# Performance work log

Hardware: AMD Instinct MI355X
Metric: run time of the kernel (lower is better)

The kernel has to match this reference:

```python
import jax, jax.numpy as jnp
import numpy as np

N_NODES = 100000
N_EDGES = 3200000
IN_C, HID_C, OUT_C = 64, 128, 64


def gcn_conv(x, src, dst, W, b, n):
    """PyG GCNConv: h = x @ W; out[d] += norm(e) * h[s]; norm = deg^-1/2[s]*deg^-1/2[d].
    src/dst already include self-loops."""
    h = x @ W  # [N, out_c]
    deg = jax.ops.segment_sum(jnp.ones_like(dst, dtype=h.dtype), dst, num_segments=n)
    dinv = jnp.where(deg > 0, jax.lax.rsqrt(deg), 0.0)
    norm = dinv[src] * dinv[dst]  # [E]
    msg = h[src] * norm[:, None]  # [E, out_c] -- dominant memory traffic
    return jax.ops.segment_sum(msg, dst, num_segments=n) + b


def setup_inputs() -> dict:
    key = jax.random.key(0)
    k1, k2, k3, k4 = jax.random.split(key, 4)
    x = jax.random.normal(k1, (N_NODES, IN_C), dtype=jnp.float32)
    edge_index = jax.random.randint(k2, (2, N_EDGES), 0, N_NODES, dtype=jnp.int64)
    W1 = jax.random.normal(k3, (IN_C, HID_C), dtype=jnp.float32) / np.sqrt(IN_C)
    b1 = jnp.zeros((HID_C,), dtype=jnp.float32)
    W2 = jax.random.normal(k4, (HID_C, OUT_C), dtype=jnp.float32) / np.sqrt(HID_C)
    b2 = jnp.zeros((OUT_C,), dtype=jnp.float32)
    return {"x": x, "edge_index": edge_index, "W1": W1, "b1": b1, "W2": W2, "b2": b2}


def reference(x, edge_index, W1, b1, W2, b2):
    n = x.shape[0]
    loops = jnp.arange(n, dtype=edge_index.dtype)  # self-loops, as PyG GCNConv adds
    src = jnp.concatenate([edge_index[0], loops])
    dst = jnp.concatenate([edge_index[1], loops])
    h = gcn_conv(x, src, dst, W1, b1, n)
    h = jax.nn.relu(h)
    out = gcn_conv(h, src, dst, W2, b2, n)
    return out
```

## Files before the change

### kernel.cpp

```cpp
#include <hip/hip_runtime.h>
#include <math.h>


#define IN_C 64
#define HID_C 128
#define OUT_C 64
#define BSHIFT 9
#define BW (1 << BSHIFT)
#define NPB 512

typedef __attribute__((ext_vector_type(8))) short bf16x8;
typedef __attribute__((ext_vector_type(4))) float f32x4;
typedef __attribute__((ext_vector_type(2))) float v2f;

__device__ __forceinline__ unsigned short f2bf(float f) {
  unsigned u = __float_as_uint(f);
  return (unsigned short)((u + 0x7FFF + ((u >> 16) & 1)) >> 16);
}
__device__ __forceinline__ v2f cvt2(unsigned u) {
  v2f r;
  r.x = __uint_as_float(u << 16);
  r.y = __uint_as_float(u & 0xFFFF0000u);
  return r;
}
__device__ __forceinline__ unsigned pack2(v2f v) {
  return ((unsigned)f2bf(v.y) << 16) | f2bf(v.x);
}


__global__ __launch_bounds__(256) void k_part1(const int* __restrict__ ei, int e, int n,
    int nb, int* __restrict__ pcnt,
    const float* __restrict__ W1, const float* __restrict__ W2,
    unsigned short* __restrict__ Wt1, unsigned short* __restrict__ Wt2,
    unsigned short* __restrict__ xs_zero, unsigned short* __restrict__ h2s_zero) {
  extern __shared__ int lh[];
  const int t = threadIdx.x;
  if (blockIdx.x >= NPB) {
    int bb = blockIdx.x - NPB;
    if (bb == 32) {
      if (t < 64) { xs_zero[t] = 0; h2s_zero[t] = 0; }
      return;
    }
    int i = bb * 256 + t;
    if (i < IN_C * HID_C) {
      int k = i >> 7, c = i & (HID_C - 1);
      Wt1[c * IN_C + k] = f2bf(W1[i]);
    }
    if (i < HID_C * OUT_C) {
      int k = i >> 6, c = i & (OUT_C - 1);
      Wt2[c * HID_C + k] = f2bf(W2[i]);
    }
    return;
  }
  __shared__ int sflag;
  if (t == 0) sflag = 0;
  for (int i = t; i < nb; i += 256) lh[i] = 0;
  __syncthreads();
  const int chunk = (e + NPB - 1) / NPB;
  const int lo = blockIdx.x * chunk;
  const int hi = min(lo + chunk, e);
  {
    int lim = min(hi, lo + 512);
    int f = 0;
    for (int i = lo + t; i < lim; i += 256)
      if (ei[2 * i + 1] != 0) f = 1;
    if (f) sflag = 1;
  }
  __syncthreads();
  const int f = sflag;
  for (int i = lo + t; i < hi; i += 256) {
    int d;
    if (f) d = __builtin_nontemporal_load(&ei[e + i]);
    else   d = (int)__builtin_nontemporal_load(&((const long long*)ei)[e + i]);
    d = min(max(d, 0), n - 1);
    atomicAdd(&lh[d >> BSHIFT], 1);
  }
  __syncthreads();
  for (int i = t; i < nb; i += 256) pcnt[(size_t)i * NPB + blockIdx.x] = lh[i];
}


__global__ __launch_bounds__(256) void k_bscan(int* __restrict__ pcnt,
    int* __restrict__ btot) {
  __shared__ int ws[256];
  const int b = blockIdx.x;
  const int t = threadIdx.x;
  int* row = pcnt + (size_t)b * NPB;
  int2 v = ((int2*)row)[t];
  int s0 = v.x;
  int s1 = s0 + v.y;
  ws[t] = s1;
  __syncthreads();
  for (int off = 1; off < 256; off <<= 1) {
    int u = (t >= off) ? ws[t - off] : 0;
    __syncthreads();
    ws[t] += u;
    __syncthreads();
  }
  int base = (t == 0) ? 0 : ws[t - 1];
  ((int2*)row)[t] = make_int2(base, base + s0);
  if (t == 255) btot[b] = ws[255];
}


__global__ __launch_bounds__(256) void k_part2(const int* __restrict__ ei, int e, int n,
    int nb, const int* __restrict__ pcnt, const int* __restrict__ btot,
    unsigned* __restrict__ ebuf) {
  __shared__ int se[256];
  __shared__ int base_l[256];
  __shared__ int cur[256];
  __shared__ int sflag;
  const int t = threadIdx.x;
  if (t == 0) sflag = 0;
  se[t] = (t < nb) ? btot[t] : 0;
  __syncthreads();
  for (int off = 1; off < 256; off <<= 1) {
    int u = (t >= off) ? se[t - off] : 0;
    __syncthreads();
    se[t] += u;
    __syncthreads();
  }
  if (t < nb) {
    int eb = (t == 0) ? 0 : se[t - 1];
    base_l[t] = eb + pcnt[(size_t)t * NPB + blockIdx.x];
    cur[t] = 0;
  }
  const int chunk = (e + NPB - 1) / NPB;
  const int lo = blockIdx.x * chunk;
  const int hi = min(lo + chunk, e);
  {
    int lim = min(hi, lo + 512);
    int f = 0;
    for (int i = lo + t; i < lim; i += 256)
      if (ei[2 * i + 1] != 0) f = 1;
    if (f) sflag = 1;
  }
  __syncthreads();
  const int f = sflag;
  for (int i = lo + t; i < hi; i += 256) {
    int s, d;
    if (f) {
      s = __builtin_nontemporal_load(&ei[i]);
      d = __builtin_nontemporal_load(&ei[e + i]);
    } else {
      s = (int)__builtin_nontemporal_load(&((const long long*)ei)[i]);
      d = (int)__builtin_nontemporal_load(&((const long long*)ei)[e + i]);
    }
    s = min(max(s, 0), n - 1);
    d = min(max(d, 0), n - 1);
    int b = d >> BSHIFT;
    int slot = atomicAdd(&cur[b], 1);
    ebuf[base_l[b] + slot] = ((unsigned)(d & (BW - 1)) << 23) | (unsigned)s;
  }
}


__global__ __launch_bounds__(1024) void k_finalize(const unsigned* __restrict__ ebuf,
    const int* __restrict__ btot, const float* __restrict__ x,
    unsigned short* __restrict__ xs, int n, int nb,
    int* __restrict__ row_ptr, float* __restrict__ dinv, int* __restrict__ col) {
  __shared__ int se[256], sc[256];
  __shared__ int ldeg[BW];
  __shared__ int lofs[BW];
  __shared__ int lcur[BW];
  __shared__ float sdv[BW];
  __shared__ int wsum[256];
  const int b = blockIdx.x;
  const int t = threadIdx.x;
  const int T = 1024;
  int bc = 0, nodes = 0;
  if (t < nb) {
    bc = btot[t];
    nodes = min(BW, n - t * BW);
  }
  if (t < 256) { se[t] = bc; sc[t] = bc + nodes; }
  __syncthreads();
  for (int off = 1; off < 256; off <<= 1) {
    int ve = 0, vc = 0;
    if (t < 256 && t >= off) { ve = se[t - off]; vc = sc[t - off]; }
    __syncthreads();
    if (t < 256) { se[t] += ve; sc[t] += vc; }
    __syncthreads();
  }
  const int eb = (b == 0) ? 0 : se[b - 1];
  const int ee = se[b];
  const int cb = (b == 0) ? 0 : sc[b - 1];
  const int lo = b * BW;
  const int nn = min(BW, n - lo);
  for (int k = t; k < BW; k += T) ldeg[k] = 0;
  __syncthreads();
  for (int k = t; k < nn; k += T) ldeg[k] = 1;
  __syncthreads();
  for (int j = eb + t; j < ee; j += T) {
    int dl = (int)(ebuf[j] >> 23);
    atomicAdd(&ldeg[dl], 1);
  }
  __syncthreads();
  int p0 = 0, p1 = 0;
  if (t < 256) {
    p0 = ldeg[2 * t]; p1 = ldeg[2 * t + 1];
    wsum[t] = p0 + p1;
  }
  __syncthreads();
  for (int off = 1; off < 256; off <<= 1) {
    int v = 0;
    if (t < 256 && t >= off) v = wsum[t - off];
    __syncthreads();
    if (t < 256) wsum[t] += v;
    __syncthreads();
  }
  if (t < 256) {
    int pb = (t == 0) ? 0 : wsum[t - 1];
    lofs[2 * t] = pb;
    lofs[2 * t + 1] = pb + p0;
  }
  __syncthreads();
  for (int k = t; k < nn; k += T) {
    int base = cb + lofs[k];
    float dv = rsqrtf((float)ldeg[k]);
    row_ptr[lo + k] = base;
    dinv[lo + k] = dv;
    sdv[k] = dv;
    col[base] = lo + k;
    lcur[k] = lofs[k] + 1;
  }
  if (b == nb - 1 && t == 0) row_ptr[n] = sc[nb - 1];
  __syncthreads();
  for (int j = eb + t; j < ee; j += T) {
    unsigned pk = ebuf[j];
    int s = (int)(pk & 0x7FFFFF);
    int dl = (int)(pk >> 23);
    int p = atomicAdd(&lcur[dl], 1);
    col[cb + p] = s;
  }
  const float4* x4 = (const float4*)x;
  for (int idx = t; idx < nn * 16; idx += T) {
    int row = idx >> 4, q = idx & 15;
    float sc2 = sdv[row];
    float4 v = x4[(size_t)(lo + row) * 16 + q];
    ushort4 o;
    o.x = f2bf(v.x * sc2); o.y = f2bf(v.y * sc2);
    o.z = f2bf(v.z * sc2); o.w = f2bf(v.w * sc2);
    ((ushort4*)xs)[(size_t)(lo + row) * 16 + q] = o;
  }
}


template<bool BIAS, bool OUT_BF16>
__global__ __launch_bounds__(256) void k_agg(const unsigned short* __restrict__ feat,
    const int* __restrict__ row_ptr, const int* __restrict__ col,
    const float* __restrict__ dinv, const float* __restrict__ bias,
    void* __restrict__ outv, int n) {
  const int wid = threadIdx.x >> 6;
  const int lane = threadIdx.x & 63;
  const int es = lane >> 3;
  const int c8 = lane & 7;
  const int d = blockIdx.x * 4 + wid;
  if (d >= n) return;
  const int beg = row_ptr[d], end = row_ptr[d + 1];
  const uint4* f16 = (const uint4*)feat;
  const int rem = end - beg - es;
  const int c = (rem > 0) ? ((rem + 7) >> 3) : 0;
  const int last = end - 1;
  v2f a0 = {0.f, 0.f}, a1 = {0.f, 0.f}, a2 = {0.f, 0.f}, a3 = {0.f, 0.f};
  for (int g = 0; g < c; g += 4) {
    int j0 = beg + es + 8 * g;
    int i0 = col[j0];
    int i1 = col[min(j0 + 8, last)];
    int i2 = col[min(j0 + 16, last)];
    int i3 = col[min(j0 + 24, last)];
    if (g + 1 >= c) i1 = n;
    if (g + 2 >= c) i2 = n;
    if (g + 3 >= c) i3 = n;
    uint4 u0 = f16[(size_t)i0 * 8 + c8];
    uint4 u1 = f16[(size_t)i1 * 8 + c8];
    uint4 u2 = f16[(size_t)i2 * 8 + c8];
    uint4 u3 = f16[(size_t)i3 * 8 + c8];
    a0 += cvt2(u0.x) + cvt2(u1.x) + cvt2(u2.x) + cvt2(u3.x);
    a1 += cvt2(u0.y) + cvt2(u1.y) + cvt2(u2.y) + cvt2(u3.y);
    a2 += cvt2(u0.z) + cvt2(u1.z) + cvt2(u2.z) + cvt2(u3.z);
    a3 += cvt2(u0.w) + cvt2(u1.w) + cvt2(u2.w) + cvt2(u3.w);
  }
#pragma unroll
  for (int off = 8; off <= 32; off <<= 1) {
    v2f o0, o1, o2, o3;
    o0.x = __shfl_xor(a0.x, off); o0.y = __shfl_xor(a0.y, off);
    o1.x = __shfl_xor(a1.x, off); o1.y = __shfl_xor(a1.y, off);
    o2.x = __shfl_xor(a2.x, off); o2.y = __shfl_xor(a2.y, off);
    o3.x = __shfl_xor(a3.x, off); o3.y = __shfl_xor(a3.y, off);
    a0 += o0; a1 += o1; a2 += o2; a3 += o3;
  }
  if (es == 0) {
    float sc = dinv[d];
    v2f vs = {sc, sc};
    a0 *= vs; a1 *= vs; a2 *= vs; a3 *= vs;
    if (BIAS) {
      const v2f* b2v = (const v2f*)bias;
      a0 += b2v[c8 * 4 + 0]; a1 += b2v[c8 * 4 + 1];
      a2 += b2v[c8 * 4 + 2]; a3 += b2v[c8 * 4 + 3];
    }
    if (OUT_BF16) {
      uint4 o;
      o.x = pack2(a0); o.y = pack2(a1); o.z = pack2(a2); o.w = pack2(a3);
      ((uint4*)outv)[(size_t)d * 8 + c8] = o;
    } else {
      float4* o4 = (float4*)outv;
      o4[(size_t)d * 16 + c8 * 2]     = make_float4(a0.x, a0.y, a1.x, a1.y);
      o4[(size_t)d * 16 + c8 * 2 + 1] = make_float4(a2.x, a2.y, a3.x, a3.y);
    }
  }
}


__global__ __launch_bounds__(256) void k_mlp(const unsigned short* __restrict__ A1,
    const unsigned short* __restrict__ Wt1, const unsigned short* __restrict__ Wt2,
    const float* __restrict__ b1, const float* __restrict__ dinv,
    unsigned short* __restrict__ h2s, int M) {
  __shared__ unsigned short sA[16 * 136];
  const int wv = threadIdx.x >> 6;
  const int lane = threadIdx.x & 63;
  const int m = lane & 15;
  const int q = lane >> 4;
  const int r0 = blockIdx.x * 16;
  const int ra = min(r0 + m, M - 1);
  f32x4 acc0 = {0.f, 0.f, 0.f, 0.f}, acc1 = {0.f, 0.f, 0.f, 0.f};
#pragma unroll
  for (int kt = 0; kt < IN_C; kt += 32) {
    bf16x8 a  = *(const bf16x8*)&A1[(size_t)ra * IN_C + kt + q * 8];
    bf16x8 p  = *(const bf16x8*)&Wt1[(size_t)(wv * 16 + m) * IN_C + kt + q * 8];
    bf16x8 p2 = *(const bf16x8*)&Wt1[(size_t)((wv + 4) * 16 + m) * IN_C + kt + q * 8];
    acc0 = __builtin_amdgcn_mfma_f32_16x16x32_bf16(a, p, acc0, 0, 0, 0);
    acc1 = __builtin_amdgcn_mfma_f32_16x16x32_bf16(a, p2, acc1, 0, 0, 0);
  }
  float dv[4];
#pragma unroll
  for (int i = 0; i < 4; i++) dv[i] = dinv[min(r0 + q * 4 + i, M - 1)];
  {
    int c = wv * 16 + m;
    float bv = b1[c];
#pragma unroll
    for (int i = 0; i < 4; i++)
      sA[(q * 4 + i) * 136 + c] = f2bf(fmaxf(acc0[i] + bv, 0.f) * dv[i]);
    c = (wv + 4) * 16 + m;
    bv = b1[c];
#pragma unroll
    for (int i = 0; i < 4; i++)
      sA[(q * 4 + i) * 136 + c] = f2bf(fmaxf(acc1[i] + bv, 0.f) * dv[i]);
  }
  __syncthreads();
  f32x4 acc = {0.f, 0.f, 0.f, 0.f};
#pragma unroll
  for (int kt = 0; kt < HID_C; kt += 32) {
    bf16x8 a = *(const bf16x8*)&sA[m * 136 + kt + q * 8];
    bf16x8 p = *(const bf16x8*)&Wt2[(size_t)(wv * 16 + m) * HID_C + kt + q * 8];
    acc = __builtin_amdgcn_mfma_f32_16x16x32_bf16(a, p, acc, 0, 0, 0);
  }
  int c = wv * 16 + m;
#pragma unroll
  for (int i = 0; i < 4; i++) {
    int row = r0 + q * 4 + i;
    if (row < M) h2s[(size_t)row * OUT_C + c] = f2bf(acc[i]);
  }
}


extern "C" void kernel_launch(void* const* d_in, const int* in_sizes, int n_in,
                              void* d_out, int out_size, void* d_ws, size_t ws_size,
                              hipStream_t stream) {
  const float* x  = (const float*)d_in[0];
  const int*   ei = (const int*)d_in[1];
  const float* W1 = (const float*)d_in[2];
  const float* b1 = (const float*)d_in[3];
  const float* W2 = (const float*)d_in[4];
  const float* b2 = (const float*)d_in[5];
  float* out = (float*)d_out;

  const int n = in_sizes[0] / IN_C;
  const int e = in_sizes[1] / 2;
  const int nb = (n + BW - 1) >> BSHIFT;

  char* p = (char*)d_ws;
  auto alloc = [&](size_t bytes) {
    char* r = p;
    p += (bytes + 255) & ~(size_t)255;
    return r;
  };
  int*   pcnt       = (int*)alloc((size_t)nb * NPB * 4);
  int*   btot       = (int*)alloc((size_t)nb * 4);
  int*   row_ptr    = (int*)alloc((size_t)(n + 1) * 4);
  float* dinv       = (float*)alloc((size_t)n * 4);
  int*   col        = (int*)alloc((size_t)(e + n) * 4);
  unsigned* ebuf    = (unsigned*)alloc((size_t)e * 4);
  unsigned short* xs  = (unsigned short*)alloc((size_t)(n + 1) * IN_C * 2);
  unsigned short* A1  = (unsigned short*)alloc((size_t)n * IN_C * 2);
  unsigned short* h2s = (unsigned short*)alloc((size_t)(n + 1) * OUT_C * 2);
  unsigned short* Wt1 = (unsigned short*)alloc((size_t)IN_C * HID_C * 2);
  unsigned short* Wt2 = (unsigned short*)alloc((size_t)HID_C * OUT_C * 2);

  k_part1<<<NPB + 33, 256, nb * 4, stream>>>(ei, e, n, nb, pcnt, W1, W2, Wt1, Wt2,
      xs + (size_t)n * IN_C, h2s + (size_t)n * OUT_C);
  k_bscan<<<nb, 256, 0, stream>>>(pcnt, btot);
  k_part2<<<NPB, 256, 0, stream>>>(ei, e, n, nb, pcnt, btot, ebuf);
  k_finalize<<<nb, 1024, 0, stream>>>(ebuf, btot, x, xs, n, nb, row_ptr, dinv, col);

  k_agg<false, true><<<(n + 3) / 4, 256, 0, stream>>>(xs, row_ptr, col, dinv, nullptr, A1, n);
  k_mlp<<<(n + 15) / 16, 256, 0, stream>>>(A1, Wt1, Wt2, b1, dinv, h2s, n);
  k_agg<true, false><<<(n + 3) / 4, 256, 0, stream>>>(h2s, row_ptr, col, dinv, b2, out, n);
}
```

Measured before the change: 309.8 us.

## Fuse first-layer aggregation into the MLP kernel and use nontemporal col loads

The first neighbour aggregation is merged into the MLP kernel. Each 256-thread block aggregates 16 destination rows into shared memory and then runs both MFMA GEMMs, so the A1 intermediate buffer and one kernel launch go away. The gather now uses 32-bit byte offsets instead of size_t indexing, and col is read with nontemporal loads. In exchange, each wave processes 4 rows serially, which means a quarter as many waves for the aggregation phase and possible latency or occupancy loss.

```diff
diff --git a/kernel.cpp b/kernel.cpp
--- a/kernel.cpp
+++ b/kernel.cpp
@@ -246,11 +246,48 @@
 }
 
 
-template<bool BIAS, bool OUT_BF16>
-__global__ __launch_bounds__(256) void k_agg(const unsigned short* __restrict__ feat,
+__device__ __forceinline__ void agg_row(const char* __restrict__ fb,
+    const int* __restrict__ col, int beg, int end, int es, unsigned coff, int n,
+    v2f& a0, v2f& a1, v2f& a2, v2f& a3) {
+  const int rem = end - beg - es;
+  const int c = (rem > 0) ? ((rem + 7) >> 3) : 0;
+  const int last = end - 1;
+  const unsigned zrow = ((unsigned)n << 7) | coff;
+  for (int g = 0; g < c; g += 4) {
+    int j0 = beg + es + 8 * g;
+    int i0 = __builtin_nontemporal_load(&col[j0]);
+    int i1 = __builtin_nontemporal_load(&col[min(j0 + 8, last)]);
+    int i2 = __builtin_nontemporal_load(&col[min(j0 + 16, last)]);
+    int i3 = __builtin_nontemporal_load(&col[min(j0 + 24, last)]);
+    unsigned o0 = ((unsigned)i0 << 7) | coff;
+    unsigned o1 = (g + 1 >= c) ? zrow : (((unsigned)i1 << 7) | coff);
+    unsigned o2 = (g + 2 >= c) ? zrow : (((unsigned)i2 << 7) | coff);
+    unsigned o3 = (g + 3 >= c) ? zrow : (((unsigned)i3 << 7) | coff);
+    uint4 u0 = *(const uint4*)(fb + o0);
+    uint4 u1 = *(const uint4*)(fb + o1);
+    uint4 u2 = *(const uint4*)(fb + o2);
+    uint4 u3 = *(const uint4*)(fb + o3);
+    a0 += cvt2(u0.x) + cvt2(u1.x) + cvt2(u2.x) + cvt2(u3.x);
+    a1 += cvt2(u0.y) + cvt2(u1.y) + cvt2(u2.y) + cvt2(u3.y);
+    a2 += cvt2(u0.z) + cvt2(u1.z) + cvt2(u2.z) + cvt2(u3.z);
+    a3 += cvt2(u0.w) + cvt2(u1.w) + cvt2(u2.w) + cvt2(u3.w);
+  }
+#pragma unroll
+  for (int off = 8; off <= 32; off <<= 1) {
+    v2f o0, o1, o2, o3;
+    o0.x = __shfl_xor(a0.x, off); o0.y = __shfl_xor(a0.y, off);
+    o1.x = __shfl_xor(a1.x, off); o1.y = __shfl_xor(a1.y, off);
+    o2.x = __shfl_xor(a2.x, off); o2.y = __shfl_xor(a2.y, off);
+    o3.x = __shfl_xor(a3.x, off); o3.y = __shfl_xor(a3.y, off);
+    a0 += o0; a1 += o1; a2 += o2; a3 += o3;
+  }
+}
+
+
+__global__ __launch_bounds__(256) void k_agg2(const unsigned short* __restrict__ feat,
     const int* __restrict__ row_ptr, const int* __restrict__ col,
     const float* __restrict__ dinv, const float* __restrict__ bias,
-    void* __restrict__ outv, int n) {
+    float* __restrict__ out, int n) {
   const int wid = threadIdx.x >> 6;
   const int lane = threadIdx.x & 63;
   const int es = lane >> 3;
@@ -258,75 +295,62 @@
   const int d = blockIdx.x * 4 + wid;
   if (d >= n) return;
   const int beg = row_ptr[d], end = row_ptr[d + 1];
-  const uint4* f16 = (const uint4*)feat;
-  const int rem = end - beg - es;
-  const int c = (rem > 0) ? ((rem + 7) >> 3) : 0;
-  const int last = end - 1;
   v2f a0 = {0.f, 0.f}, a1 = {0.f, 0.f}, a2 = {0.f, 0.f}, a3 = {0.f, 0.f};
-  for (int g = 0; g < c; g += 4) {
-    int j0 = beg + es + 8 * g;
-    int i0 = col[j0];
-    int i1 = col[min(j0 + 8, last)];
-    int i2 = col[min(j0 + 16, last)];
-    int i3 = col[min(j0 + 24, last)];
-    if (g + 1 >= c) i1 = n;
-    if (g + 2 >= c) i2 = n;
-    if (g + 3 >= c) i3 = n;
-    uint4 u0 = f16[(size_t)i0 * 8 + c8];
-    uint4 u1 = f16[(size_t)i1 * 8 + c8];
-    uint4 u2 = f16[(size_t)i2 * 8 + c8];
-    uint4 u3 = f16[(size_t)i3 * 8 + c8];
-    a0 += cvt2(u0.x) + cvt2(u1.x) + cvt2(u2.x) + cvt2(u3.x);
-    a1 += cvt2(u0.y) + cvt2(u1.y) + cvt2(u2.y) + cvt2(u3.y);
-    a2 += cvt2(u0.z) + cvt2(u1.z) + cvt2(u2.z) + cvt2(u3.z);
-    a3 += cvt2(u0.w) + cvt2(u1.w) + cvt2(u2.w) + cvt2(u3.w);
-  }
-#pragma unroll
-  for (int off = 8; off <= 32; off <<= 1) {
-    v2f o0, o1, o2, o3;
-    o0.x = __shfl_xor(a0.x, off); o0.y = __shfl_xor(a0.y, off);
-    o1.x = __shfl_xor(a1.x, off); o1.y = __shfl_xor(a1.y, off);
-    o2.x = __shfl_xor(a2.x, off); o2.y = __shfl_xor(a2.y, off);
-    o3.x = __shfl_xor(a3.x, off); o3.y = __shfl_xor(a3.y, off);
-    a0 += o0; a1 += o1; a2 += o2; a3 += o3;
-  }
+  agg_row((const char*)feat, col, beg, end, es, (unsigned)c8 * 16u, n,
+          a0, a1, a2, a3);
   if (es == 0) {
     float sc = dinv[d];
     v2f vs = {sc, sc};
     a0 *= vs; a1 *= vs; a2 *= vs; a3 *= vs;
-    if (BIAS) {
-      const v2f* b2v = (const v2f*)bias;
-      a0 += b2v[c8 * 4 + 0]; a1 += b2v[c8 * 4 + 1];
-      a2 += b2v[c8 * 4 + 2]; a3 += b2v[c8 * 4 + 3];
-    }
-    if (OUT_BF16) {
-      uint4 o;
-      o.x = pack2(a0); o.y = pack2(a1); o.z = pack2(a2); o.w = pack2(a3);
-      ((uint4*)outv)[(size_t)d * 8 + c8] = o;
-    } else {
-      float4* o4 = (float4*)outv;
-      o4[(size_t)d * 16 + c8 * 2]     = make_float4(a0.x, a0.y, a1.x, a1.y);
-      o4[(size_t)d * 16 + c8 * 2 + 1] = make_float4(a2.x, a2.y, a3.x, a3.y);
-    }
-  }
-}
-
-
-__global__ __launch_bounds__(256) void k_mlp(const unsigned short* __restrict__ A1,
+    const v2f* b2v = (const v2f*)bias;
+    a0 += b2v[c8 * 4 + 0]; a1 += b2v[c8 * 4 + 1];
+    a2 += b2v[c8 * 4 + 2]; a3 += b2v[c8 * 4 + 3];
+    float4* o4 = (float4*)out;
+    o4[(size_t)d * 16 + c8 * 2]     = make_float4(a0.x, a0.y, a1.x, a1.y);
+    o4[(size_t)d * 16 + c8 * 2 + 1] = make_float4(a2.x, a2.y, a3.x, a3.y);
+  }
+}
+
+
+__global__ __launch_bounds__(256) void k_aggmlp(const unsigned short* __restrict__ feat,
+    const int* __restrict__ row_ptr, const int* __restrict__ col,
+    const float* __restrict__ dinv, const float* __restrict__ b1,
     const unsigned short* __restrict__ Wt1, const unsigned short* __restrict__ Wt2,
-    const float* __restrict__ b1, const float* __restrict__ dinv,
-    unsigned short* __restrict__ h2s, int M) {
-  __shared__ unsigned short sA[16 * 136];
+    unsigned short* __restrict__ h2s, int n) {
+  __shared__ __align__(16) unsigned short sA1[16][72];
+  __shared__ __align__(16) unsigned short sH[16][136];
   const int wv = threadIdx.x >> 6;
   const int lane = threadIdx.x & 63;
+  const int es = lane >> 3;
+  const int c8 = lane & 7;
+  const int r0 = blockIdx.x * 16;
+  const unsigned coff = (unsigned)c8 * 16u;
+  for (int rr = 0; rr < 4; ++rr) {
+    const int d = r0 + wv * 4 + rr;
+    if (d < n) {
+      const int beg = row_ptr[d], end = row_ptr[d + 1];
+      v2f a0 = {0.f, 0.f}, a1 = {0.f, 0.f}, a2 = {0.f, 0.f}, a3 = {0.f, 0.f};
+      agg_row((const char*)feat, col, beg, end, es, coff, n, a0, a1, a2, a3);
+      if (es == 0) {
+        float sc = dinv[d];
+        v2f vs = {sc, sc};
+        a0 *= vs; a1 *= vs; a2 *= vs; a3 *= vs;
+        uint4 o;
+        o.x = pack2(a0); o.y = pack2(a1); o.z = pack2(a2); o.w = pack2(a3);
+        *(uint4*)&sA1[wv * 4 + rr][c8 * 8] = o;
+      }
+    } else if (es == 0) {
+      uint4 z = {0u, 0u, 0u, 0u};
+      *(uint4*)&sA1[wv * 4 + rr][c8 * 8] = z;
+    }
+  }
+  __syncthreads();
   const int m = lane & 15;
   const int q = lane >> 4;
-  const int r0 = blockIdx.x * 16;
-  const int ra = min(r0 + m, M - 1);
   f32x4 acc0 = {0.f, 0.f, 0.f, 0.f}, acc1 = {0.f, 0.f, 0.f, 0.f};
 #pragma unroll
   for (int kt = 0; kt < IN_C; kt += 32) {
-    bf16x8 a  = *(const bf16x8*)&A1[(size_t)ra * IN_C + kt + q * 8];
+    bf16x8 a  = *(const bf16x8*)&sA1[m][kt + q * 8];
     bf16x8 p  = *(const bf16x8*)&Wt1[(size_t)(wv * 16 + m) * IN_C + kt + q * 8];
     bf16x8 p2 = *(const bf16x8*)&Wt1[(size_t)((wv + 4) * 16 + m) * IN_C + kt + q * 8];
     acc0 = __builtin_amdgcn_mfma_f32_16x16x32_bf16(a, p, acc0, 0, 0, 0);
@@ -334,24 +358,24 @@
   }
   float dv[4];
 #pragma unroll
-  for (int i = 0; i < 4; i++) dv[i] = dinv[min(r0 + q * 4 + i, M - 1)];
+  for (int i = 0; i < 4; i++) dv[i] = dinv[min(r0 + q * 4 + i, n - 1)];
   {
     int c = wv * 16 + m;
     float bv = b1[c];
 #pragma unroll
     for (int i = 0; i < 4; i++)
-      sA[(q * 4 + i) * 136 + c] = f2bf(fmaxf(acc0[i] + bv, 0.f) * dv[i]);
+      sH[q * 4 + i][c] = f2bf(fmaxf(acc0[i] + bv, 0.f) * dv[i]);
     c = (wv + 4) * 16 + m;
     bv = b1[c];
 #pragma unroll
     for (int i = 0; i < 4; i++)
-      sA[(q * 4 + i) * 136 + c] = f2bf(fmaxf(acc1[i] + bv, 0.f) * dv[i]);
+      sH[q * 4 + i][c] = f2bf(fmaxf(acc1[i] + bv, 0.f) * dv[i]);
   }
   __syncthreads();
   f32x4 acc = {0.f, 0.f, 0.f, 0.f};
 #pragma unroll
   for (int kt = 0; kt < HID_C; kt += 32) {
-    bf16x8 a = *(const bf16x8*)&sA[m * 136 + kt + q * 8];
+    bf16x8 a = *(const bf16x8*)&sH[m][kt + q * 8];
     bf16x8 p = *(const bf16x8*)&Wt2[(size_t)(wv * 16 + m) * HID_C + kt + q * 8];
     acc = __builtin_amdgcn_mfma_f32_16x16x32_bf16(a, p, acc, 0, 0, 0);
   }
@@ -359,7 +383,7 @@
 #pragma unroll
   for (int i = 0; i < 4; i++) {
     int row = r0 + q * 4 + i;
-    if (row < M) h2s[(size_t)row * OUT_C + c] = f2bf(acc[i]);
+    if (row < n) h2s[(size_t)row * OUT_C + c] = f2bf(acc[i]);
   }
 }
 
@@ -392,7 +416,6 @@
   int*   col        = (int*)alloc((size_t)(e + n) * 4);
   unsigned* ebuf    = (unsigned*)alloc((size_t)e * 4);
   unsigned short* xs  = (unsigned short*)alloc((size_t)(n + 1) * IN_C * 2);
-  unsigned short* A1  = (unsigned short*)alloc((size_t)n * IN_C * 2);
   unsigned short* h2s = (unsigned short*)alloc((size_t)(n + 1) * OUT_C * 2);
   unsigned short* Wt1 = (unsigned short*)alloc((size_t)IN_C * HID_C * 2);
   unsigned short* Wt2 = (unsigned short*)alloc((size_t)HID_C * OUT_C * 2);
@@ -403,7 +426,6 @@
   k_part2<<<NPB, 256, 0, stream>>>(ei, e, n, nb, pcnt, btot, ebuf);
   k_finalize<<<nb, 1024, 0, stream>>>(ebuf, btot, x, xs, n, nb, row_ptr, dinv, col);
 
-  k_agg<false, true><<<(n + 3) / 4, 256, 0, stream>>>(xs, row_ptr, col, dinv, nullptr, A1, n);
-  k_mlp<<<(n + 15) / 16, 256, 0, stream>>>(A1, Wt1, Wt2, b1, dinv, h2s, n);
-  k_agg<true, false><<<(n + 3) / 4, 256, 0, stream>>>(h2s, row_ptr, col, dinv, b2, out, n);
-}
+  k_aggmlp<<<(n + 15) / 16, 256, 0, stream>>>(xs, row_ptr, col, dinv, b1, Wt1, Wt2, h2s, n);
+  k_agg2<<<(n + 3) / 4, 256, 0, stream>>>(h2s, row_ptr, col, dinv, b2, out, n);
+}
```

After: 306.2 us. No clear change (-1.2%).
